# Performance work log

Hardware: AMD Instinct MI355X
Metric: run time of the kernel (lower is better)

Reference implementation:

```python
import jax, jax.numpy as jnp
import numpy as np

POOL_SIZE = 4
MAX_DIM = 256
GRID = MAX_DIM // POOL_SIZE  # 64
N_VOX = GRID ** 3            # 262144
N = 1_000_000
C = 64


def setup_inputs() -> dict:
    key = jax.random.key(0)
    k1, k2 = jax.random.split(key)
    vertices = jax.random.randint(k1, (N, 3), 0, MAX_DIM, dtype=jnp.int64)
    features = jax.random.normal(k2, (N, C), dtype=jnp.float32)
    return {"vertices": vertices, "features": features}


def reference(vertices, features):
    # floor-divide coords into voxel grid
    v = vertices // POOL_SIZE                      # [N,3] in [0, GRID)
    vox = v[:, 0] * (GRID * GRID) + v[:, 1] * GRID + v[:, 2]  # [N] flat voxel id
    # amax-pool features per voxel (empty voxels get -inf identity)
    pooled = jax.ops.segment_max(features, vox, num_segments=N_VOX)  # [N_VOX, C]
    # voxels with no points must be 0 (torch output_features initialized to zeros)
    counts = jax.ops.segment_sum(jnp.ones((vertices.shape[0],), jnp.int32), vox,
                                 num_segments=N_VOX)
    out = jnp.where((counts > 0)[:, None], pooled, jnp.zeros((), features.dtype))
    return out.reshape(-1)  # [N_VOX * C]
```

## Files before the change

### kernel.cpp

```cpp
#include <hip/hip_runtime.h>

#define GRID 64
#define N_VOX (GRID * GRID * GRID)
#define NCH 64


typedef float f32x4 __attribute__((ext_vector_type(4)));
typedef int   i32x4 __attribute__((ext_vector_type(4)));

__device__ __forceinline__ int vox_of(int x, int y, int z) {
    return ((x >> 2) << 12) | ((y >> 2) << 6) | (z >> 2);
}

__device__ __forceinline__ float4 max4(float4 a, float4 b) {
    float4 r;
    r.x = fmaxf(a.x, b.x); r.y = fmaxf(a.y, b.y);
    r.z = fmaxf(a.z, b.z); r.w = fmaxf(a.w, b.w);
    return r;
}

__device__ __forceinline__ float4 ntload4(const float4* p) {
    f32x4 v = __builtin_nontemporal_load((const f32x4*)p);
    return make_float4(v[0], v[1], v[2], v[3]);
}
__device__ __forceinline__ void ntstore4(float4* p, float4 v) {
    f32x4 t; t[0] = v.x; t[1] = v.y; t[2] = v.z; t[3] = v.w;
    __builtin_nontemporal_store(t, (f32x4*)p);
}
__device__ __forceinline__ int4 ntload_i4(const int4* p) {
    i32x4 v = __builtin_nontemporal_load((const i32x4*)p);
    return make_int4(v[0], v[1], v[2], v[3]);
}

__global__ void k_hist(const int* __restrict__ verts, int* __restrict__ vox,
                       int* __restrict__ rank, int* __restrict__ counts, int n) {
    int t  = blockIdx.x * blockDim.x + threadIdx.x;
    int p0 = t * 4;
    if (p0 >= n) return;

    if (p0 + 4 <= n) {
        const int4* v4 = (const int4*)verts;
        int4 a = ntload_i4(&v4[3 * t + 0]);
        int4 b = ntload_i4(&v4[3 * t + 1]);
        int4 c = ntload_i4(&v4[3 * t + 2]);
        int w0 = vox_of(a.x, a.y, a.z);
        int w1 = vox_of(a.w, b.x, b.y);
        int w2 = vox_of(b.z, b.w, c.x);
        int w3 = vox_of(c.y, c.z, c.w);
        ((int4*)vox)[t] = make_int4(w0, w1, w2, w3);
        int r0 = atomicAdd(&counts[w0], 1);
        int r1 = atomicAdd(&counts[w1], 1);
        int r2 = atomicAdd(&counts[w2], 1);
        int r3 = atomicAdd(&counts[w3], 1);
        ((int4*)rank)[t] = make_int4(r0, r1, r2, r3);
    } else {
        for (int p = p0; p < n; p++) {
            int w = vox_of(verts[3 * p], verts[3 * p + 1], verts[3 * p + 2]);
            vox[p]  = w;
            rank[p] = atomicAdd(&counts[w], 1);
        }
    }
}

__global__ void __launch_bounds__(256)
k_bsum(const int* __restrict__ counts, int* __restrict__ bsum) {
    int b = blockIdx.x;
    int t = threadIdx.x;
    int4 c = ((const int4*)counts)[b * 256 + t];
    int s = c.x + c.y + c.z + c.w;
    #pragma unroll
    for (int off = 32; off; off >>= 1) s += __shfl_down(s, off);
    __shared__ int ws[4];
    int lane = t & 63, wid = t >> 6;
    if (lane == 0) ws[wid] = s;
    __syncthreads();
    if (t == 0) bsum[b] = ws[0] + ws[1] + ws[2] + ws[3];
}

__global__ void __launch_bounds__(256) k_scan2(int* __restrict__ bsum) {
    int t = threadIdx.x;
    int v = bsum[t];
    int lane = t & 63;
    int wid  = t >> 6;
    int incl = v;
    #pragma unroll
    for (int off = 1; off < 64; off <<= 1) {
        int u = __shfl_up(incl, off);
        if (lane >= off) incl += u;
    }
    __shared__ int ws[4];
    if (lane == 63) ws[wid] = incl;
    __syncthreads();
    int base = 0;
    for (int i = 0; i < wid; i++) base += ws[i];
    bsum[t] = base + incl - v;
}

__global__ void __launch_bounds__(1024)
k_scanfinal(const int* __restrict__ counts, const int* __restrict__ bsum,
            int* __restrict__ gstart) {
    int g = blockIdx.x * 1024 + threadIdx.x;
    int v = counts[g];
    int lane = threadIdx.x & 63;
    int wid  = threadIdx.x >> 6;

    int incl = v;
    #pragma unroll
    for (int off = 1; off < 64; off <<= 1) {
        int u = __shfl_up(incl, off);
        if (lane >= off) incl += u;
    }
    __shared__ int wsum[16];
    if (lane == 63) wsum[wid] = incl;
    __syncthreads();
    if (wid == 0) {
        int s  = (lane < 16) ? wsum[lane] : 0;
        int si = s;
        #pragma unroll
        for (int off = 1; off < 16; off <<= 1) {
            int u = __shfl_up(si, off);
            if (lane >= off) si += u;
        }
        if (lane < 16) wsum[lane] = si - s;
    }
    __syncthreads();

    int start = bsum[blockIdx.x] + wsum[wid] + incl - v;
    gstart[g] = start;
    if (g == N_VOX - 1) gstart[N_VOX] = start + v;
}

__global__ void k_scatter_idx(const int* __restrict__ vox,
                              const int* __restrict__ rank,
                              const int* __restrict__ gstart,
                              int* __restrict__ sorted_idx, int n) {
    int t  = blockIdx.x * blockDim.x + threadIdx.x;
    int p0 = t * 4;
    if (p0 >= n) return;

    if (p0 + 4 <= n) {
        int4 w = ((const int4*)vox)[t];
        int4 r = ((const int4*)rank)[t];
        sorted_idx[gstart[w.x] + r.x] = p0 + 0;
        sorted_idx[gstart[w.y] + r.y] = p0 + 1;
        sorted_idx[gstart[w.z] + r.z] = p0 + 2;
        sorted_idx[gstart[w.w] + r.w] = p0 + 3;
    } else {
        for (int p = p0; p < n; p++)
            sorted_idx[gstart[vox[p]] + rank[p]] = p;
    }
}

#define VPB 16
#define IDX_CAP 2048

__global__ void __launch_bounds__(256)
k_gather(const int* __restrict__ sorted_idx,
         const int* __restrict__ gstart,
         const float4* __restrict__ feats4,
         float4* __restrict__ out4) {
    __shared__ int sst[VPB + 1];
    __shared__ int sidx[IDX_CAP];

    int vox0 = blockIdx.x * VPB;
    if (threadIdx.x < VPB + 1) sst[threadIdx.x] = gstart[vox0 + threadIdx.x];
    __syncthreads();

    int bstart = sst[0];
    int span   = sst[VPB] - bstart;
    bool fits  = (span <= IDX_CAP);
    if (fits) {
        for (int i = threadIdx.x; i < span; i += 256)
            sidx[i] = sorted_idx[bstart + i];
    }
    __syncthreads();

    int g   = threadIdx.x >> 4;
    int sub = threadIdx.x & 15;
    int s0  = sst[g];
    int cnt = sst[g + 1] - s0;
    float4* outp = &out4[(size_t)(vox0 + g) * 16 + sub];

    if (cnt == 0) {
        ntstore4(outp, make_float4(0.f, 0.f, 0.f, 0.f));
        return;
    }

    int off = s0 - bstart;
    float4 a0 = make_float4(-INFINITY, -INFINITY, -INFINITY, -INFINITY);
    float4 a1 = a0, a2 = a0, a3 = a0;

    for (int j = 0; j < cnt; j += 4) {
        int j1 = min(j + 1, cnt - 1);
        int j2 = min(j + 2, cnt - 1);
        int j3 = min(j + 3, cnt - 1);
        int p0, p1, p2, p3;
        if (fits) {
            p0 = sidx[off + j];  p1 = sidx[off + j1];
            p2 = sidx[off + j2]; p3 = sidx[off + j3];
        } else {
            p0 = sorted_idx[s0 + j];  p1 = sorted_idx[s0 + j1];
            p2 = sorted_idx[s0 + j2]; p3 = sorted_idx[s0 + j3];
        }
        float4 f0 = ntload4(&feats4[(size_t)p0 * 16 + sub]);
        float4 f1 = ntload4(&feats4[(size_t)p1 * 16 + sub]);
        float4 f2 = ntload4(&feats4[(size_t)p2 * 16 + sub]);
        float4 f3 = ntload4(&feats4[(size_t)p3 * 16 + sub]);
        a0 = max4(a0, f0);
        a1 = max4(a1, f1);
        a2 = max4(a2, f2);
        a3 = max4(a3, f3);
    }
    ntstore4(outp, max4(max4(a0, a1), max4(a2, a3)));
}

extern "C" void kernel_launch(void* const* d_in, const int* in_sizes, int n_in,
                              void* d_out, int out_size, void* d_ws, size_t ws_size,
                              hipStream_t stream) {
    const int*   verts = (const int*)d_in[0];
    const float* feats = (const float*)d_in[1];
    float*       out   = (float*)d_out;

    const int n_pts = in_sizes[0] / 3;

    char* w = (char*)d_ws;
    int*  vox        = (int*)w;              w += (size_t)n_pts * 4;
    int*  rank       = (int*)w;              w += (size_t)n_pts * 4;
    int*  sorted_idx = (int*)w;              w += (size_t)n_pts * 4;
    int*  counts     = (int*)w;              w += (size_t)N_VOX * 4;
    int*  gstart     = (int*)w;              w += (size_t)(N_VOX + 16) * 4;
    int*  bsum       = (int*)w;

    hipMemsetAsync(counts, 0, (size_t)N_VOX * 4, stream);

    {
        const int block = 256;
        const int nthr  = (n_pts + 3) / 4;
        const int grid  = (nthr + block - 1) / block;
        k_hist<<<grid, block, 0, stream>>>(verts, vox, rank, counts, n_pts);
    }
    k_bsum<<<256, 256, 0, stream>>>(counts, bsum);
    k_scan2<<<1, 256, 0, stream>>>(bsum);
    k_scanfinal<<<N_VOX / 1024, 1024, 0, stream>>>(counts, bsum, gstart);

    {
        const int block = 256;
        const int nthr  = (n_pts + 3) / 4;
        const int grid  = (nthr + block - 1) / block;
        k_scatter_idx<<<grid, block, 0, stream>>>(vox, rank, gstart,
                                                  sorted_idx, n_pts);
    }
    {
        const int block = 256;
        const int grid  = N_VOX / VPB;
        k_gather<<<grid, block, 0, stream>>>(sorted_idx, gstart,
                                             (const float4*)feats, (float4*)out);
    }
}
```

Measured before the change: 425.3 us.

## Replace three-kernel scan with single-pass decoupled look-back scan; widen per-thread work

Merges the block-sum, block-scan and final-scan kernels into one single-pass kernel. It uses a ticket counter and per-chunk aggregate/prefix flags (decoupled look-back), which removes two kernel launches and a round trip through counts. The histogram and scatter kernels now handle 8 points per thread instead of 4. The gather loop drops the duplicate clamped loads and uses a scalar remainder loop instead. This relies on spin-waiting across blocks and on the state buffers being zeroed by the extended memset.

Result: no change. 433.2 us (+1.9%).

```diff
diff --git a/kernel.cpp b/kernel.cpp
--- a/kernel.cpp
+++ b/kernel.cpp
@@ -3,6 +3,7 @@
 #define GRID 64
 #define N_VOX (GRID * GRID * GRID)
 #define NCH 64
+#define NCHUNK 256
 
 
 typedef float f32x4 __attribute__((ext_vector_type(4)));
@@ -35,24 +36,37 @@
 __global__ void k_hist(const int* __restrict__ verts, int* __restrict__ vox,
                        int* __restrict__ rank, int* __restrict__ counts, int n) {
     int t  = blockIdx.x * blockDim.x + threadIdx.x;
-    int p0 = t * 4;
+    int p0 = t * 8;
     if (p0 >= n) return;
 
-    if (p0 + 4 <= n) {
+    if (p0 + 8 <= n) {
         const int4* v4 = (const int4*)verts;
-        int4 a = ntload_i4(&v4[3 * t + 0]);
-        int4 b = ntload_i4(&v4[3 * t + 1]);
-        int4 c = ntload_i4(&v4[3 * t + 2]);
+        int4 a = ntload_i4(&v4[6 * t + 0]);
+        int4 b = ntload_i4(&v4[6 * t + 1]);
+        int4 c = ntload_i4(&v4[6 * t + 2]);
+        int4 d = ntload_i4(&v4[6 * t + 3]);
+        int4 e = ntload_i4(&v4[6 * t + 4]);
+        int4 f = ntload_i4(&v4[6 * t + 5]);
         int w0 = vox_of(a.x, a.y, a.z);
         int w1 = vox_of(a.w, b.x, b.y);
         int w2 = vox_of(b.z, b.w, c.x);
         int w3 = vox_of(c.y, c.z, c.w);
-        ((int4*)vox)[t] = make_int4(w0, w1, w2, w3);
+        int w4 = vox_of(d.x, d.y, d.z);
+        int w5 = vox_of(d.w, e.x, e.y);
+        int w6 = vox_of(e.z, e.w, f.x);
+        int w7 = vox_of(f.y, f.z, f.w);
+        ((int4*)vox)[2 * t + 0] = make_int4(w0, w1, w2, w3);
+        ((int4*)vox)[2 * t + 1] = make_int4(w4, w5, w6, w7);
         int r0 = atomicAdd(&counts[w0], 1);
         int r1 = atomicAdd(&counts[w1], 1);
         int r2 = atomicAdd(&counts[w2], 1);
         int r3 = atomicAdd(&counts[w3], 1);
-        ((int4*)rank)[t] = make_int4(r0, r1, r2, r3);
+        int r4 = atomicAdd(&counts[w4], 1);
+        int r5 = atomicAdd(&counts[w5], 1);
+        int r6 = atomicAdd(&counts[w6], 1);
+        int r7 = atomicAdd(&counts[w7], 1);
+        ((int4*)rank)[2 * t + 0] = make_int4(r0, r1, r2, r3);
+        ((int4*)rank)[2 * t + 1] = make_int4(r4, r5, r6, r7);
     } else {
         for (int p = p0; p < n; p++) {
             int w = vox_of(verts[3 * p], verts[3 * p + 1], verts[3 * p + 2]);
@@ -63,71 +77,76 @@
 }
 
 __global__ void __launch_bounds__(256)
-k_bsum(const int* __restrict__ counts, int* __restrict__ bsum) {
-    int b = blockIdx.x;
-    int t = threadIdx.x;
+k_scan(const int* __restrict__ counts, int* __restrict__ gstart,
+       unsigned long long* __restrict__ state, int* __restrict__ ticket) {
+    __shared__ int s_ticket;
+    __shared__ int wbase[4];
+    __shared__ int s_base;
+
+    if (threadIdx.x == 0) s_ticket = atomicAdd(ticket, 1);
+    __syncthreads();
+    const int b    = s_ticket;
+    const int t    = threadIdx.x;
+    const int lane = t & 63;
+    const int wid  = t >> 6;
+
     int4 c = ((const int4*)counts)[b * 256 + t];
     int s = c.x + c.y + c.z + c.w;
-    #pragma unroll
-    for (int off = 32; off; off >>= 1) s += __shfl_down(s, off);
-    __shared__ int ws[4];
-    int lane = t & 63, wid = t >> 6;
-    if (lane == 0) ws[wid] = s;
-    __syncthreads();
-    if (t == 0) bsum[b] = ws[0] + ws[1] + ws[2] + ws[3];
-}
-
-__global__ void __launch_bounds__(256) k_scan2(int* __restrict__ bsum) {
-    int t = threadIdx.x;
-    int v = bsum[t];
-    int lane = t & 63;
-    int wid  = t >> 6;
-    int incl = v;
+
+    int incl = s;
     #pragma unroll
     for (int off = 1; off < 64; off <<= 1) {
         int u = __shfl_up(incl, off);
         if (lane >= off) incl += u;
     }
-    __shared__ int ws[4];
-    if (lane == 63) ws[wid] = incl;
-    __syncthreads();
-    int base = 0;
-    for (int i = 0; i < wid; i++) base += ws[i];
-    bsum[t] = base + incl - v;
-}
-
-__global__ void __launch_bounds__(1024)
-k_scanfinal(const int* __restrict__ counts, const int* __restrict__ bsum,
-            int* __restrict__ gstart) {
-    int g = blockIdx.x * 1024 + threadIdx.x;
-    int v = counts[g];
-    int lane = threadIdx.x & 63;
-    int wid  = threadIdx.x >> 6;
-
-    int incl = v;
-    #pragma unroll
-    for (int off = 1; off < 64; off <<= 1) {
-        int u = __shfl_up(incl, off);
-        if (lane >= off) incl += u;
-    }
-    __shared__ int wsum[16];
-    if (lane == 63) wsum[wid] = incl;
-    __syncthreads();
+    if (lane == 63) wbase[wid] = incl;
+    __syncthreads();
+
     if (wid == 0) {
-        int s  = (lane < 16) ? wsum[lane] : 0;
-        int si = s;
-        #pragma unroll
-        for (int off = 1; off < 16; off <<= 1) {
-            int u = __shfl_up(si, off);
-            if (lane >= off) si += u;
-        }
-        if (lane < 16) wsum[lane] = si - s;
-    }
-    __syncthreads();
-
-    int start = bsum[blockIdx.x] + wsum[wid] + incl - v;
-    gstart[g] = start;
-    if (g == N_VOX - 1) gstart[N_VOX] = start + v;
+        int agg = wbase[0] + wbase[1] + wbase[2] + wbase[3];
+        if (lane == 0) {
+            __hip_atomic_store(&state[b], (1ULL << 32) | (unsigned)agg,
+                               __ATOMIC_RELEASE, __HIP_MEMORY_SCOPE_AGENT);
+        }
+        int excl = 0;
+        int p_hi = b - 1;
+        while (p_hi >= 0) {
+            int p = p_hi - lane;
+            unsigned long long v;
+            do {
+                v = (p >= 0)
+                  ? __hip_atomic_load(&state[p], __ATOMIC_ACQUIRE,
+                                      __HIP_MEMORY_SCOPE_AGENT)
+                  : (2ULL << 32);
+            } while (__any((int)((v >> 32) == 0)));
+            unsigned long long m = __ballot((int)((v >> 32) == 2));
+            int cut = m ? (__ffsll((long long)m) - 1) : 64;
+            int contrib = (lane <= cut) ? (int)(unsigned)v : 0;
+            #pragma unroll
+            for (int o = 32; o; o >>= 1) contrib += __shfl_down(contrib, o);
+            excl += __shfl(contrib, 0);
+            if (m) break;
+            p_hi -= 64;
+        }
+        if (lane == 0) {
+            int agg2 = wbase[0] + wbase[1] + wbase[2] + wbase[3];
+            __hip_atomic_store(&state[b], (2ULL << 32) | (unsigned)(excl + agg2),
+                               __ATOMIC_RELEASE, __HIP_MEMORY_SCOPE_AGENT);
+            s_base = excl;
+            if (b == NCHUNK - 1) gstart[N_VOX] = excl + agg2;
+        }
+    }
+    __syncthreads();
+
+    int wexcl = 0;
+    for (int i = 0; i < wid; i++) wexcl += wbase[i];
+    int base = s_base + wexcl + (incl - s);
+    int4 g;
+    g.x = base;
+    g.y = base + c.x;
+    g.z = base + c.x + c.y;
+    g.w = base + c.x + c.y + c.z;
+    ((int4*)gstart)[b * 256 + t] = g;
 }
 
 __global__ void k_scatter_idx(const int* __restrict__ vox,
@@ -135,16 +154,22 @@
                               const int* __restrict__ gstart,
                               int* __restrict__ sorted_idx, int n) {
     int t  = blockIdx.x * blockDim.x + threadIdx.x;
-    int p0 = t * 4;
+    int p0 = t * 8;
     if (p0 >= n) return;
 
-    if (p0 + 4 <= n) {
-        int4 w = ((const int4*)vox)[t];
-        int4 r = ((const int4*)rank)[t];
-        sorted_idx[gstart[w.x] + r.x] = p0 + 0;
-        sorted_idx[gstart[w.y] + r.y] = p0 + 1;
-        sorted_idx[gstart[w.z] + r.z] = p0 + 2;
-        sorted_idx[gstart[w.w] + r.w] = p0 + 3;
+    if (p0 + 8 <= n) {
+        int4 w0 = ((const int4*)vox)[2 * t + 0];
+        int4 w1 = ((const int4*)vox)[2 * t + 1];
+        int4 r0 = ((const int4*)rank)[2 * t + 0];
+        int4 r1 = ((const int4*)rank)[2 * t + 1];
+        sorted_idx[gstart[w0.x] + r0.x] = p0 + 0;
+        sorted_idx[gstart[w0.y] + r0.y] = p0 + 1;
+        sorted_idx[gstart[w0.z] + r0.z] = p0 + 2;
+        sorted_idx[gstart[w0.w] + r0.w] = p0 + 3;
+        sorted_idx[gstart[w1.x] + r1.x] = p0 + 4;
+        sorted_idx[gstart[w1.y] + r1.y] = p0 + 5;
+        sorted_idx[gstart[w1.z] + r1.z] = p0 + 6;
+        sorted_idx[gstart[w1.w] + r1.w] = p0 + 7;
     } else {
         for (int p = p0; p < n; p++)
             sorted_idx[gstart[vox[p]] + rank[p]] = p;
@@ -190,26 +215,24 @@
     float4 a0 = make_float4(-INFINITY, -INFINITY, -INFINITY, -INFINITY);
     float4 a1 = a0, a2 = a0, a3 = a0;
 
-    for (int j = 0; j < cnt; j += 4) {
-        int j1 = min(j + 1, cnt - 1);
-        int j2 = min(j + 2, cnt - 1);
-        int j3 = min(j + 3, cnt - 1);
+    int j = 0;
+    for (; j + 4 <= cnt; j += 4) {
         int p0, p1, p2, p3;
         if (fits) {
-            p0 = sidx[off + j];  p1 = sidx[off + j1];
-            p2 = sidx[off + j2]; p3 = sidx[off + j3];
+            p0 = sidx[off + j];     p1 = sidx[off + j + 1];
+            p2 = sidx[off + j + 2]; p3 = sidx[off + j + 3];
         } else {
-            p0 = sorted_idx[s0 + j];  p1 = sorted_idx[s0 + j1];
-            p2 = sorted_idx[s0 + j2]; p3 = sorted_idx[s0 + j3];
-        }
-        float4 f0 = ntload4(&feats4[(size_t)p0 * 16 + sub]);
-        float4 f1 = ntload4(&feats4[(size_t)p1 * 16 + sub]);
-        float4 f2 = ntload4(&feats4[(size_t)p2 * 16 + sub]);
-        float4 f3 = ntload4(&feats4[(size_t)p3 * 16 + sub]);
-        a0 = max4(a0, f0);
-        a1 = max4(a1, f1);
-        a2 = max4(a2, f2);
-        a3 = max4(a3, f3);
+            p0 = sorted_idx[s0 + j];     p1 = sorted_idx[s0 + j + 1];
+            p2 = sorted_idx[s0 + j + 2]; p3 = sorted_idx[s0 + j + 3];
+        }
+        a0 = max4(a0, ntload4(&feats4[(size_t)p0 * 16 + sub]));
+        a1 = max4(a1, ntload4(&feats4[(size_t)p1 * 16 + sub]));
+        a2 = max4(a2, ntload4(&feats4[(size_t)p2 * 16 + sub]));
+        a3 = max4(a3, ntload4(&feats4[(size_t)p3 * 16 + sub]));
+    }
+    for (; j < cnt; j++) {
+        int p = fits ? sidx[off + j] : sorted_idx[s0 + j];
+        a0 = max4(a0, ntload4(&feats4[(size_t)p * 16 + sub]));
     }
     ntstore4(outp, max4(max4(a0, a1), max4(a2, a3)));
 }
@@ -228,24 +251,24 @@
     int*  rank       = (int*)w;              w += (size_t)n_pts * 4;
     int*  sorted_idx = (int*)w;              w += (size_t)n_pts * 4;
     int*  counts     = (int*)w;              w += (size_t)N_VOX * 4;
-    int*  gstart     = (int*)w;              w += (size_t)(N_VOX + 16) * 4;
-    int*  bsum       = (int*)w;
-
-    hipMemsetAsync(counts, 0, (size_t)N_VOX * 4, stream);
+    unsigned long long* state = (unsigned long long*)w;  w += (size_t)NCHUNK * 8;
+    int*  ticket     = (int*)w;              w += 16;
+    const size_t zero_bytes = (size_t)N_VOX * 4 + (size_t)NCHUNK * 8 + 16;
+    int*  gstart     = (int*)w;              w += (size_t)(N_VOX + 4) * 4;
+
+    hipMemsetAsync(counts, 0, zero_bytes, stream);
 
     {
         const int block = 256;
-        const int nthr  = (n_pts + 3) / 4;
+        const int nthr  = (n_pts + 7) / 8;
         const int grid  = (nthr + block - 1) / block;
         k_hist<<<grid, block, 0, stream>>>(verts, vox, rank, counts, n_pts);
     }
-    k_bsum<<<256, 256, 0, stream>>>(counts, bsum);
-    k_scan2<<<1, 256, 0, stream>>>(bsum);
-    k_scanfinal<<<N_VOX / 1024, 1024, 0, stream>>>(counts, bsum, gstart);
+    k_scan<<<NCHUNK, 256, 0, stream>>>(counts, gstart, state, ticket);
 
     {
         const int block = 256;
-        const int nthr  = (n_pts + 3) / 4;
+        const int nthr  = (n_pts + 7) / 8;
         const int grid  = (nthr + block - 1) / block;
         k_scatter_idx<<<grid, block, 0, stream>>>(vox, rank, gstart,
                                                   sorted_idx, n_pts);
```

## Fuse histogram, scan, scatter and gather into one cooperative persistent kernel

Applied to the files above, without the earlier changes.

Replaces the memset and six separate kernel launches with one cooperative kernel of 1024 blocks, using grid-wide syncs between the count, block-scan, partial-scan, start-offset, index-scatter and max-gather phases. The goal is to remove launch gaps and the memset. In exchange it adds five grid barriers and runs the gather phase as a persistent loop over tiles with fewer resident threads. It also drops the clamped duplicate loads in the gather loop in favour of a scalar tail loop.

New measurement: 1.054 ms. +147.8%, slower.

```diff
diff --git a/kernel.cpp b/kernel.cpp
--- a/kernel.cpp
+++ b/kernel.cpp
@@ -1,8 +1,16 @@
 #include <hip/hip_runtime.h>
+#include <hip/hip_cooperative_groups.h>
+
+namespace cg = cooperative_groups;
 
 #define GRID 64
 #define N_VOX (GRID * GRID * GRID)
 #define NCH 64
+#define NBLK 1024
+#define TPB 256
+#define NTHR (NBLK * TPB)
+#define TILES_PER_BLK (N_VOX / 16 / NBLK)
+#define IDX_CAP 2048
 
 
 typedef float f32x4 __attribute__((ext_vector_type(4)));
@@ -32,228 +40,192 @@
     return make_int4(v[0], v[1], v[2], v[3]);
 }
 
-__global__ void k_hist(const int* __restrict__ verts, int* __restrict__ vox,
-                       int* __restrict__ rank, int* __restrict__ counts, int n) {
-    int t  = blockIdx.x * blockDim.x + threadIdx.x;
-    int p0 = t * 4;
-    if (p0 >= n) return;
-
-    if (p0 + 4 <= n) {
-        const int4* v4 = (const int4*)verts;
-        int4 a = ntload_i4(&v4[3 * t + 0]);
-        int4 b = ntload_i4(&v4[3 * t + 1]);
-        int4 c = ntload_i4(&v4[3 * t + 2]);
-        int w0 = vox_of(a.x, a.y, a.z);
-        int w1 = vox_of(a.w, b.x, b.y);
-        int w2 = vox_of(b.z, b.w, c.x);
-        int w3 = vox_of(c.y, c.z, c.w);
-        ((int4*)vox)[t] = make_int4(w0, w1, w2, w3);
-        int r0 = atomicAdd(&counts[w0], 1);
-        int r1 = atomicAdd(&counts[w1], 1);
-        int r2 = atomicAdd(&counts[w2], 1);
-        int r3 = atomicAdd(&counts[w3], 1);
-        ((int4*)rank)[t] = make_int4(r0, r1, r2, r3);
-    } else {
-        for (int p = p0; p < n; p++) {
-            int w = vox_of(verts[3 * p], verts[3 * p + 1], verts[3 * p + 2]);
-            vox[p]  = w;
-            rank[p] = atomicAdd(&counts[w], 1);
-        }
-    }
-}
-
-__global__ void __launch_bounds__(256)
-k_bsum(const int* __restrict__ counts, int* __restrict__ bsum) {
-    int b = blockIdx.x;
-    int t = threadIdx.x;
-    int4 c = ((const int4*)counts)[b * 256 + t];
-    int s = c.x + c.y + c.z + c.w;
-    #pragma unroll
-    for (int off = 32; off; off >>= 1) s += __shfl_down(s, off);
-    __shared__ int ws[4];
-    int lane = t & 63, wid = t >> 6;
-    if (lane == 0) ws[wid] = s;
-    __syncthreads();
-    if (t == 0) bsum[b] = ws[0] + ws[1] + ws[2] + ws[3];
-}
-
-__global__ void __launch_bounds__(256) k_scan2(int* __restrict__ bsum) {
-    int t = threadIdx.x;
-    int v = bsum[t];
-    int lane = t & 63;
-    int wid  = t >> 6;
-    int incl = v;
-    #pragma unroll
-    for (int off = 1; off < 64; off <<= 1) {
-        int u = __shfl_up(incl, off);
-        if (lane >= off) incl += u;
-    }
-    __shared__ int ws[4];
-    if (lane == 63) ws[wid] = incl;
-    __syncthreads();
-    int base = 0;
-    for (int i = 0; i < wid; i++) base += ws[i];
-    bsum[t] = base + incl - v;
-}
-
-__global__ void __launch_bounds__(1024)
-k_scanfinal(const int* __restrict__ counts, const int* __restrict__ bsum,
-            int* __restrict__ gstart) {
-    int g = blockIdx.x * 1024 + threadIdx.x;
-    int v = counts[g];
-    int lane = threadIdx.x & 63;
-    int wid  = threadIdx.x >> 6;
-
-    int incl = v;
-    #pragma unroll
-    for (int off = 1; off < 64; off <<= 1) {
-        int u = __shfl_up(incl, off);
-        if (lane >= off) incl += u;
-    }
-    __shared__ int wsum[16];
-    if (lane == 63) wsum[wid] = incl;
-    __syncthreads();
-    if (wid == 0) {
-        int s  = (lane < 16) ? wsum[lane] : 0;
-        int si = s;
+__global__ void __launch_bounds__(TPB, 4)
+k_fused(const int* __restrict__ verts, const float4* __restrict__ feats4,
+        float4* __restrict__ out4,
+        int* __restrict__ vox, int* __restrict__ rank,
+        int* __restrict__ sorted_idx, int* __restrict__ counts,
+        int* __restrict__ gstart, int* __restrict__ partial,
+        int* __restrict__ pbase, int n) {
+    cg::grid_group gg = cg::this_grid();
+    const int B    = blockIdx.x;
+    const int t    = threadIdx.x;
+    const int gtid = B * TPB + t;
+    const int lane = t & 63;
+    const int wid  = t >> 6;
+
+    __shared__ int sh_wb[4];
+    __shared__ int sh_sst[17];
+    __shared__ int sh_sidx[IDX_CAP];
+
+    counts[gtid] = 0;
+    gg.sync();
+
+    for (int q = gtid; q * 4 < n; q += NTHR) {
+        int p0 = q * 4;
+        if (p0 + 4 <= n) {
+            const int4* v4 = (const int4*)verts;
+            int4 a = ntload_i4(&v4[3 * q + 0]);
+            int4 b = ntload_i4(&v4[3 * q + 1]);
+            int4 c = ntload_i4(&v4[3 * q + 2]);
+            int w0 = vox_of(a.x, a.y, a.z);
+            int w1 = vox_of(a.w, b.x, b.y);
+            int w2 = vox_of(b.z, b.w, c.x);
+            int w3 = vox_of(c.y, c.z, c.w);
+            ((int4*)vox)[q] = make_int4(w0, w1, w2, w3);
+            int r0 = atomicAdd(&counts[w0], 1);
+            int r1 = atomicAdd(&counts[w1], 1);
+            int r2 = atomicAdd(&counts[w2], 1);
+            int r3 = atomicAdd(&counts[w3], 1);
+            ((int4*)rank)[q] = make_int4(r0, r1, r2, r3);
+        } else {
+            for (int p = p0; p < n; p++) {
+                int w = vox_of(verts[3 * p], verts[3 * p + 1], verts[3 * p + 2]);
+                vox[p]  = w;
+                rank[p] = atomicAdd(&counts[w], 1);
+            }
+        }
+    }
+    gg.sync();
+
+    int lex;
+    {
+        int v    = counts[gtid];
+        int incl = v;
         #pragma unroll
-        for (int off = 1; off < 16; off <<= 1) {
-            int u = __shfl_up(si, off);
-            if (lane >= off) si += u;
-        }
-        if (lane < 16) wsum[lane] = si - s;
-    }
-    __syncthreads();
-
-    int start = bsum[blockIdx.x] + wsum[wid] + incl - v;
-    gstart[g] = start;
-    if (g == N_VOX - 1) gstart[N_VOX] = start + v;
-}
-
-__global__ void k_scatter_idx(const int* __restrict__ vox,
-                              const int* __restrict__ rank,
-                              const int* __restrict__ gstart,
-                              int* __restrict__ sorted_idx, int n) {
-    int t  = blockIdx.x * blockDim.x + threadIdx.x;
-    int p0 = t * 4;
-    if (p0 >= n) return;
-
-    if (p0 + 4 <= n) {
-        int4 w = ((const int4*)vox)[t];
-        int4 r = ((const int4*)rank)[t];
-        sorted_idx[gstart[w.x] + r.x] = p0 + 0;
-        sorted_idx[gstart[w.y] + r.y] = p0 + 1;
-        sorted_idx[gstart[w.z] + r.z] = p0 + 2;
-        sorted_idx[gstart[w.w] + r.w] = p0 + 3;
-    } else {
-        for (int p = p0; p < n; p++)
-            sorted_idx[gstart[vox[p]] + rank[p]] = p;
-    }
-}
-
-#define VPB 16
-#define IDX_CAP 2048
-
-__global__ void __launch_bounds__(256)
-k_gather(const int* __restrict__ sorted_idx,
-         const int* __restrict__ gstart,
-         const float4* __restrict__ feats4,
-         float4* __restrict__ out4) {
-    __shared__ int sst[VPB + 1];
-    __shared__ int sidx[IDX_CAP];
-
-    int vox0 = blockIdx.x * VPB;
-    if (threadIdx.x < VPB + 1) sst[threadIdx.x] = gstart[vox0 + threadIdx.x];
-    __syncthreads();
-
-    int bstart = sst[0];
-    int span   = sst[VPB] - bstart;
-    bool fits  = (span <= IDX_CAP);
-    if (fits) {
-        for (int i = threadIdx.x; i < span; i += 256)
-            sidx[i] = sorted_idx[bstart + i];
-    }
-    __syncthreads();
-
-    int g   = threadIdx.x >> 4;
-    int sub = threadIdx.x & 15;
-    int s0  = sst[g];
-    int cnt = sst[g + 1] - s0;
-    float4* outp = &out4[(size_t)(vox0 + g) * 16 + sub];
-
-    if (cnt == 0) {
-        ntstore4(outp, make_float4(0.f, 0.f, 0.f, 0.f));
-        return;
-    }
-
-    int off = s0 - bstart;
-    float4 a0 = make_float4(-INFINITY, -INFINITY, -INFINITY, -INFINITY);
-    float4 a1 = a0, a2 = a0, a3 = a0;
-
-    for (int j = 0; j < cnt; j += 4) {
-        int j1 = min(j + 1, cnt - 1);
-        int j2 = min(j + 2, cnt - 1);
-        int j3 = min(j + 3, cnt - 1);
-        int p0, p1, p2, p3;
+        for (int off = 1; off < 64; off <<= 1) {
+            int u = __shfl_up(incl, off);
+            if (lane >= off) incl += u;
+        }
+        if (lane == 63) sh_wb[wid] = incl;
+        __syncthreads();
+        int wexcl = 0;
+        for (int i = 0; i < wid; i++) wexcl += sh_wb[i];
+        lex = wexcl + incl - v;
+        if (t == 0) partial[B] = sh_wb[0] + sh_wb[1] + sh_wb[2] + sh_wb[3];
+    }
+    gg.sync();
+
+    if (B == 0) {
+        int4 p = ((const int4*)partial)[t];
+        int s  = p.x + p.y + p.z + p.w;
+        int incl = s;
+        #pragma unroll
+        for (int off = 1; off < 64; off <<= 1) {
+            int u = __shfl_up(incl, off);
+            if (lane >= off) incl += u;
+        }
+        if (lane == 63) sh_wb[wid] = incl;
+        __syncthreads();
+        int wexcl = 0;
+        for (int i = 0; i < wid; i++) wexcl += sh_wb[i];
+        int base = wexcl + incl - s;
+        int4 e;
+        e.x = base;
+        e.y = base + p.x;
+        e.z = e.y  + p.y;
+        e.w = e.z  + p.z;
+        ((int4*)pbase)[t] = e;
+        if (t == TPB - 1) gstart[N_VOX] = base + s;
+    }
+    gg.sync();
+
+    gstart[gtid] = pbase[B] + lex;
+    gg.sync();
+
+    for (int q = gtid; q * 4 < n; q += NTHR) {
+        int p0 = q * 4;
+        if (p0 + 4 <= n) {
+            int4 w = ((const int4*)vox)[q];
+            int4 r = ((const int4*)rank)[q];
+            sorted_idx[gstart[w.x] + r.x] = p0 + 0;
+            sorted_idx[gstart[w.y] + r.y] = p0 + 1;
+            sorted_idx[gstart[w.z] + r.z] = p0 + 2;
+            sorted_idx[gstart[w.w] + r.w] = p0 + 3;
+        } else {
+            for (int p = p0; p < n; p++)
+                sorted_idx[gstart[vox[p]] + rank[p]] = p;
+        }
+    }
+    gg.sync();
+
+    const int g   = t >> 4;
+    const int sub = t & 15;
+    for (int it = 0; it < TILES_PER_BLK; ++it) {
+        int vox0 = (B * TILES_PER_BLK + it) * 16;
+        __syncthreads();
+        if (t < 17) sh_sst[t] = gstart[vox0 + t];
+        __syncthreads();
+
+        int bstart = sh_sst[0];
+        int span   = sh_sst[16] - bstart;
+        bool fits  = (span <= IDX_CAP);
         if (fits) {
-            p0 = sidx[off + j];  p1 = sidx[off + j1];
-            p2 = sidx[off + j2]; p3 = sidx[off + j3];
-        } else {
-            p0 = sorted_idx[s0 + j];  p1 = sorted_idx[s0 + j1];
-            p2 = sorted_idx[s0 + j2]; p3 = sorted_idx[s0 + j3];
-        }
-        float4 f0 = ntload4(&feats4[(size_t)p0 * 16 + sub]);
-        float4 f1 = ntload4(&feats4[(size_t)p1 * 16 + sub]);
-        float4 f2 = ntload4(&feats4[(size_t)p2 * 16 + sub]);
-        float4 f3 = ntload4(&feats4[(size_t)p3 * 16 + sub]);
-        a0 = max4(a0, f0);
-        a1 = max4(a1, f1);
-        a2 = max4(a2, f2);
-        a3 = max4(a3, f3);
-    }
-    ntstore4(outp, max4(max4(a0, a1), max4(a2, a3)));
+            for (int i = t; i < span; i += TPB)
+                sh_sidx[i] = sorted_idx[bstart + i];
+        }
+        __syncthreads();
+
+        int s0  = sh_sst[g];
+        int cnt = sh_sst[g + 1] - s0;
+        float4* outp = &out4[(size_t)(vox0 + g) * 16 + sub];
+
+        if (cnt == 0) {
+            ntstore4(outp, make_float4(0.f, 0.f, 0.f, 0.f));
+            continue;
+        }
+
+        int off = s0 - bstart;
+        float4 a0 = make_float4(-INFINITY, -INFINITY, -INFINITY, -INFINITY);
+        float4 a1 = a0, a2 = a0, a3 = a0;
+
+        int j = 0;
+        for (; j + 4 <= cnt; j += 4) {
+            int p0, p1, p2, p3;
+            if (fits) {
+                p0 = sh_sidx[off + j];     p1 = sh_sidx[off + j + 1];
+                p2 = sh_sidx[off + j + 2]; p3 = sh_sidx[off + j + 3];
+            } else {
+                p0 = sorted_idx[s0 + j];     p1 = sorted_idx[s0 + j + 1];
+                p2 = sorted_idx[s0 + j + 2]; p3 = sorted_idx[s0 + j + 3];
+            }
+            a0 = max4(a0, ntload4(&feats4[(size_t)p0 * 16 + sub]));
+            a1 = max4(a1, ntload4(&feats4[(size_t)p1 * 16 + sub]));
+            a2 = max4(a2, ntload4(&feats4[(size_t)p2 * 16 + sub]));
+            a3 = max4(a3, ntload4(&feats4[(size_t)p3 * 16 + sub]));
+        }
+        for (; j < cnt; j++) {
+            int p = fits ? sh_sidx[off + j] : sorted_idx[s0 + j];
+            a0 = max4(a0, ntload4(&feats4[(size_t)p * 16 + sub]));
+        }
+        ntstore4(outp, max4(max4(a0, a1), max4(a2, a3)));
+    }
 }
 
 extern "C" void kernel_launch(void* const* d_in, const int* in_sizes, int n_in,
                               void* d_out, int out_size, void* d_ws, size_t ws_size,
                               hipStream_t stream) {
-    const int*   verts = (const int*)d_in[0];
-    const float* feats = (const float*)d_in[1];
-    float*       out   = (float*)d_out;
-
-    const int n_pts = in_sizes[0] / 3;
+    const int*    verts  = (const int*)d_in[0];
+    const float4* feats4 = (const float4*)d_in[1];
+    float4*       out4   = (float4*)d_out;
+
+    int n_pts = in_sizes[0] / 3;
 
     char* w = (char*)d_ws;
-    int*  vox        = (int*)w;              w += (size_t)n_pts * 4;
-    int*  rank       = (int*)w;              w += (size_t)n_pts * 4;
-    int*  sorted_idx = (int*)w;              w += (size_t)n_pts * 4;
-    int*  counts     = (int*)w;              w += (size_t)N_VOX * 4;
-    int*  gstart     = (int*)w;              w += (size_t)(N_VOX + 16) * 4;
-    int*  bsum       = (int*)w;
-
-    hipMemsetAsync(counts, 0, (size_t)N_VOX * 4, stream);
-
-    {
-        const int block = 256;
-        const int nthr  = (n_pts + 3) / 4;
-        const int grid  = (nthr + block - 1) / block;
-        k_hist<<<grid, block, 0, stream>>>(verts, vox, rank, counts, n_pts);
-    }
-    k_bsum<<<256, 256, 0, stream>>>(counts, bsum);
-    k_scan2<<<1, 256, 0, stream>>>(bsum);
-    k_scanfinal<<<N_VOX / 1024, 1024, 0, stream>>>(counts, bsum, gstart);
-
-    {
-        const int block = 256;
-        const int nthr  = (n_pts + 3) / 4;
-        const int grid  = (nthr + block - 1) / block;
-        k_scatter_idx<<<grid, block, 0, stream>>>(vox, rank, gstart,
-                                                  sorted_idx, n_pts);
-    }
-    {
-        const int block = 256;
-        const int grid  = N_VOX / VPB;
-        k_gather<<<grid, block, 0, stream>>>(sorted_idx, gstart,
-                                             (const float4*)feats, (float4*)out);
-    }
-}
+    int* vox        = (int*)w;   w += (size_t)n_pts * 4;
+    int* rank       = (int*)w;   w += (size_t)n_pts * 4;
+    int* sorted_idx = (int*)w;   w += (size_t)n_pts * 4;
+    int* counts     = (int*)w;   w += (size_t)N_VOX * 4;
+    int* gstart     = (int*)w;   w += (size_t)(N_VOX + 4) * 4;
+    int* partial    = (int*)w;   w += (size_t)NBLK * 4;
+    int* pbase      = (int*)w;   w += (size_t)NBLK * 4;
+
+    void* args[] = {
+        (void*)&verts, (void*)&feats4, (void*)&out4,
+        (void*)&vox, (void*)&rank, (void*)&sorted_idx,
+        (void*)&counts, (void*)&gstart, (void*)&partial, (void*)&pbase,
+        (void*)&n_pts
+    };
+    hipLaunchCooperativeKernel((void*)k_fused, dim3(NBLK), dim3(TPB),
+                               args, 0, stream);
+}
```
